# Performance work log

Measured on AMD Instinct MI355X. Metric: run time of the kernel, lower is better.

Reference implementation:

```python
import jax, jax.numpy as jnp
import numpy as np

N = 100_000   # nodes
E = 1_600_000 # edges
IN, HID, OUT = 128, 64, 32


def _glorot(key, fan_in, fan_out):
    s = jnp.sqrt(6.0 / (fan_in + fan_out)).astype(jnp.float32)
    return jax.random.uniform(key, (fan_in, fan_out), jnp.float32, -s, s)


def setup_inputs() -> dict:
    key = jax.random.key(0)
    ks = jax.random.split(key, 8)
    x = jax.random.normal(ks[0], (N, IN), jnp.float32)
    edge_index = jax.random.randint(ks[1], (2, E), 0, N, jnp.int64)
    return {
        "x": x,
        "edge_index": edge_index,
        "W1": _glorot(ks[2], IN, HID),
        "b1": jnp.zeros((HID,), jnp.float32),
        "W_mu": _glorot(ks[3], HID, OUT),
        "b_mu": jnp.zeros((OUT,), jnp.float32),
        "W_ls": _glorot(ks[4], HID, OUT),
        "b_ls": jnp.zeros((OUT,), jnp.float32),
    }


def _gcn_conv(x, W, b, src, dst, n, dinv_sqrt):
    """PyG GCNConv: h = x @ W; symmetric-normalized scatter-add incl. self-loops; + b."""
    h = x @ W                                       # [N, F_out]
    coef = dinv_sqrt[src] * dinv_sqrt[dst]          # [E]
    msg = h[src] * coef[:, None]                    # [E, F_out] gather
    agg = jax.ops.segment_sum(msg, dst, num_segments=n)  # scatter-add
    agg = agg + h * (dinv_sqrt * dinv_sqrt)[:, None]      # self-loop contribution
    return agg + b


def reference(x, edge_index, W1, b1, W_mu, b_mu, W_ls, b_ls):
    src, dst = edge_index[0], edge_index[1]
    n = x.shape[0]
    # degree on graph with self-loops (edge weight 1), shared by all three convs
    deg = jax.ops.segment_sum(jnp.ones((src.shape[0],), x.dtype), dst, num_segments=n) + 1.0
    dinv_sqrt = jax.lax.rsqrt(deg)
    h = jax.nn.relu(_gcn_conv(x, W1, b1, src, dst, n, dinv_sqrt))
    mu = _gcn_conv(h, W_mu, b_mu, src, dst, n, dinv_sqrt)
    logstd = _gcn_conv(h, W_ls, b_ls, src, dst, n, dinv_sqrt)
    return mu, logstd
```

## Files before the change

kernel.cpp:

```cpp
#include <hip/hip_runtime.h>
#include <hip/hip_bf16.h>

#define FIN 128
#define HID 64
#define BSN 128
#define BSHIFT 7
#define SRCBITS 20
#define EPB 2048
#define BSTRIDE 2304
#define STARTBITS 21

typedef __attribute__((ext_vector_type(8))) short short8;
typedef __attribute__((ext_vector_type(4))) float floatx4;

__device__ __forceinline__ float bf2f(unsigned short u) {
    union { unsigned int i; float f; } c;
    c.i = ((unsigned int)u) << 16;
    return c.f;
}

__device__ __forceinline__ unsigned short f2bf(float f) {
    union { float f; unsigned int i; } c;
    c.f = f;
    unsigned int u = c.i;
    unsigned int r = (u + 0x7FFFu + ((u >> 16) & 1u)) >> 16;
    return (unsigned short)r;
}

__global__ __launch_bounds__(256) void bin_fill(
    const int* __restrict__ src, const int* __restrict__ dst,
    int* __restrict__ bcur, unsigned* __restrict__ rec, int E) {
    __shared__ int hist[1024];
    __shared__ int cbase[1024];
    int t = threadIdx.x;
    for (int i = t; i < 1024; i += 256) hist[i] = 0;
    __syncthreads();
    int base = blockIdx.x * EPB;
    int lim = min(base + EPB, E);
    int d[8];
#pragma unroll
    for (int k = 0; k < 8; ++k) {
        int e = base + t + k * 256;
        if (e < lim) {
            d[k] = dst[e];
            atomicAdd(&hist[d[k] >> BSHIFT], 1);
        }
    }
    __syncthreads();
    for (int b = t; b < 1024; b += 256) {
        int c = hist[b];
        cbase[b] = c ? atomicAdd(&bcur[b], c) : 0;
    }
    __syncthreads();
    for (int i = t; i < 1024; i += 256) hist[i] = 0;
    __syncthreads();
#pragma unroll
    for (int k = 0; k < 8; ++k) {
        int e = base + t + k * 256;
        if (e < lim) {
            int dd = d[k];
            int bkt = dd >> BSHIFT;
            int slot = atomicAdd(&hist[bkt], 1);
            rec[bkt * BSTRIDE + cbase[bkt] + slot] =
                (unsigned)src[e] | ((unsigned)(dd & (BSN - 1)) << SRCBITS);
        }
    }
}

__global__ void csr_build(const unsigned* __restrict__ rec, const int* __restrict__ bcur,
                          unsigned* __restrict__ rowp, int* __restrict__ csr, int N) {
    __shared__ int cnt[BSN], excl[BSN], cur[BSN];
    int b = blockIdx.x, t = threadIdx.x;
    if (t < BSN) cnt[t] = 0;
    __syncthreads();
    int base = b * BSTRIDE;
    int cb = bcur[b];
    for (int i = t; i < cb; i += 256)
        atomicAdd(&cnt[rec[base + i] >> SRCBITS], 1);
    __syncthreads();
    if (t < BSN) excl[t] = cnt[t];
    __syncthreads();
    for (int off = 1; off < BSN; off <<= 1) {
        int a = 0;
        if (t < BSN && t >= off) a = excl[t - off];
        __syncthreads();
        if (t < BSN) excl[t] += a;
        __syncthreads();
    }
    if (t < BSN) {
        int inc = excl[t];
        int ex = inc - cnt[t];
        excl[t] = ex;
        cur[t] = 0;
        int n = b * BSN + t;
        if (n < N)
            rowp[n] = (unsigned)(base + ex) | ((unsigned)cnt[t] << STARTBITS);
    }
    __syncthreads();
    for (int i = t; i < cb; i += 256) {
        unsigned r = rec[base + i];
        int dl = r >> SRCBITS;
        int slot = atomicAdd(&cur[dl], 1);
        csr[base + excl[dl] + slot] = (int)(r & ((1u << SRCBITS) - 1));
    }
}

__global__ __launch_bounds__(256) void gemm1_mfma(
    const float* __restrict__ x, const float* __restrict__ W1,
    const unsigned* __restrict__ rowp, unsigned short* __restrict__ h0, int N) {
    __shared__ unsigned short Wt[64][136];
    {
        int t = threadIdx.x;
        int k  = t >> 1;
        int c0 = (t & 1) << 5;
        const float* wr = W1 + k * HID + c0;
#pragma unroll
        for (int cc = 0; cc < 32; ++cc)
            Wt[c0 + cc][k] = f2bf(wr[cc]);
    }
    __syncthreads();
    int wave = threadIdx.x >> 6, lane = threadIdx.x & 63;
    int m = lane & 15, q = lane >> 4;
    short8 bfr[4][4];
#pragma unroll
    for (int ct = 0; ct < 4; ++ct)
#pragma unroll
        for (int kk = 0; kk < 4; ++kk)
            bfr[ct][kk] = *((const short8*)&Wt[ct * 16 + m][kk * 32 + q * 8]);
    int ntiles = N >> 4;
    for (int t = blockIdx.x * 4 + wave; t < ntiles; t += gridDim.x * 4) {
        int nbase = t << 4;
        const float* xr = x + (size_t)(nbase + m) * FIN + q * 8;
        short8 afr[4];
#pragma unroll
        for (int kk = 0; kk < 4; ++kk) {
            float4 p0 = *((const float4*)(xr + kk * 32));
            float4 p1 = *((const float4*)(xr + kk * 32 + 4));
            short8 ta;
            ta[0] = (short)f2bf(p0.x); ta[1] = (short)f2bf(p0.y);
            ta[2] = (short)f2bf(p0.z); ta[3] = (short)f2bf(p0.w);
            ta[4] = (short)f2bf(p1.x); ta[5] = (short)f2bf(p1.y);
            ta[6] = (short)f2bf(p1.z); ta[7] = (short)f2bf(p1.w);
            afr[kk] = ta;
        }
        uint4 rp = *((const uint4*)(rowp + nbase + q * 4));
        floatx4 cacc[4];
#pragma unroll
        for (int ct = 0; ct < 4; ++ct) cacc[ct] = floatx4{0.f, 0.f, 0.f, 0.f};
#pragma unroll
        for (int ct = 0; ct < 4; ++ct)
#pragma unroll
            for (int kk = 0; kk < 4; ++kk)
                cacc[ct] = __builtin_amdgcn_mfma_f32_16x16x32_bf16(afr[kk], bfr[ct][kk], cacc[ct], 0, 0, 0);
#pragma unroll
        for (int ct = 0; ct < 4; ++ct) {
#pragma unroll
            for (int r = 0; r < 4; ++r) {
                unsigned pr = (r == 0) ? rp.x : (r == 1) ? rp.y : (r == 2) ? rp.z : rp.w;
                float d = rsqrtf((float)(pr >> STARTBITS) + 1.0f);
                int n = nbase + q * 4 + r;
                h0[(size_t)n * HID + ct * 16 + m] = f2bf(cacc[ct][r] * d);
            }
        }
    }
}


#define ACC8(a, d)                                                      \
    do {                                                                \
        union { unsigned u; float f; } c_;                              \
        c_.u = (d).x << 16;          a[0] += c_.f;                      \
        c_.u = (d).x & 0xFFFF0000u;  a[1] += c_.f;                      \
        c_.u = (d).y << 16;          a[2] += c_.f;                      \
        c_.u = (d).y & 0xFFFF0000u;  a[3] += c_.f;                      \
        c_.u = (d).z << 16;          a[4] += c_.f;                      \
        c_.u = (d).z & 0xFFFF0000u;  a[5] += c_.f;                      \
        c_.u = (d).w << 16;          a[6] += c_.f;                      \
        c_.u = (d).w & 0xFFFF0000u;  a[7] += c_.f;                      \
    } while (0)

template <int MODE>
__global__ __launch_bounds__(256, 4) void pull(
    const unsigned short* __restrict__ hp,
    const unsigned* __restrict__ rowp,
    const int* __restrict__ csr,
    const float* __restrict__ b1,
    unsigned short* __restrict__ outp,
    const float* __restrict__ Wmu, const float* __restrict__ bmu,
    const float* __restrict__ Wls, const float* __restrict__ bls,
    float* __restrict__ out, int N) {
    int lane = threadIdx.x & 63;
    int wave = threadIdx.x >> 6;
    int nd8  = lane >> 3;
    int g    = lane & 7;
    int n = blockIdx.x * 32 + wave * 8 + nd8;
    bool valid = (n < N);
    int nc = valid ? n : 0;
    unsigned rp = rowp[nc];
    int start = (int)(rp & ((1u << STARTBITS) - 1u));
    int deg   = (int)(rp >> STARTBITS);
    int end   = valid ? start + deg : 0;
    if (!valid) start = 0;
    const char* hpb = (const char*)hp;
    unsigned goff = (unsigned)(g << 4);
    uint4 sv = *((const uint4*)(hpb + (((unsigned)nc) << 7) + goff));
    float di = rsqrtf((float)deg + 1.0f);
    float4 bb0 = *((const float4*)(b1 + (g << 3)));
    float4 bb1 = *((const float4*)(b1 + (g << 3) + 4));
    float a[8] = {0.f, 0.f, 0.f, 0.f, 0.f, 0.f, 0.f, 0.f};
    int j = start;
    for (; j + 8 <= end; j += 8) {
        int s0 = csr[j],     s1 = csr[j + 1], s2 = csr[j + 2], s3 = csr[j + 3];
        int s4 = csr[j + 4], s5 = csr[j + 5], s6 = csr[j + 6], s7 = csr[j + 7];
        uint4 d0 = *((const uint4*)(hpb + (((unsigned)s0) << 7) + goff));
        uint4 d1 = *((const uint4*)(hpb + (((unsigned)s1) << 7) + goff));
        uint4 d2 = *((const uint4*)(hpb + (((unsigned)s2) << 7) + goff));
        uint4 d3 = *((const uint4*)(hpb + (((unsigned)s3) << 7) + goff));
        uint4 d4 = *((const uint4*)(hpb + (((unsigned)s4) << 7) + goff));
        uint4 d5 = *((const uint4*)(hpb + (((unsigned)s5) << 7) + goff));
        uint4 d6 = *((const uint4*)(hpb + (((unsigned)s6) << 7) + goff));
        uint4 d7 = *((const uint4*)(hpb + (((unsigned)s7) << 7) + goff));
        ACC8(a, d0); ACC8(a, d1); ACC8(a, d2); ACC8(a, d3);
        ACC8(a, d4); ACC8(a, d5); ACC8(a, d6); ACC8(a, d7);
    }
    if (j + 4 <= end) {
        int s0 = csr[j], s1 = csr[j + 1], s2 = csr[j + 2], s3 = csr[j + 3];
        uint4 d0 = *((const uint4*)(hpb + (((unsigned)s0) << 7) + goff));
        uint4 d1 = *((const uint4*)(hpb + (((unsigned)s1) << 7) + goff));
        uint4 d2 = *((const uint4*)(hpb + (((unsigned)s2) << 7) + goff));
        uint4 d3 = *((const uint4*)(hpb + (((unsigned)s3) << 7) + goff));
        ACC8(a, d0); ACC8(a, d1); ACC8(a, d2); ACC8(a, d3);
        j += 4;
    }
    if (j < end) {
        int i0 = j, i1 = min(j + 1, end - 1), i2 = min(j + 2, end - 1);
        int s0 = csr[i0], s1 = csr[i1], s2 = csr[i2];
        uint4 d0 = *((const uint4*)(hpb + (((unsigned)s0) << 7) + goff));
        uint4 d1 = *((const uint4*)(hpb + (((unsigned)s1) << 7) + goff));
        uint4 d2 = *((const uint4*)(hpb + (((unsigned)s2) << 7) + goff));
        if (j + 1 >= end) { d1.x = 0u; d1.y = 0u; d1.z = 0u; d1.w = 0u; }
        if (j + 2 >= end) { d2.x = 0u; d2.y = 0u; d2.z = 0u; d2.w = 0u; }
        ACC8(a, d0); ACC8(a, d1); ACC8(a, d2);
    }
    uint4 o = {0u, 0u, 0u, 0u};
    if (valid) {
        ACC8(a, sv);
        float v[8];
        if (MODE == 0) {
            float t0;
            t0 = di * a[0] + bb0.x; v[0] = (t0 > 0.f ? t0 : 0.f) * di;
            t0 = di * a[1] + bb0.y; v[1] = (t0 > 0.f ? t0 : 0.f) * di;
            t0 = di * a[2] + bb0.z; v[2] = (t0 > 0.f ? t0 : 0.f) * di;
            t0 = di * a[3] + bb0.w; v[3] = (t0 > 0.f ? t0 : 0.f) * di;
            t0 = di * a[4] + bb1.x; v[4] = (t0 > 0.f ? t0 : 0.f) * di;
            t0 = di * a[5] + bb1.y; v[5] = (t0 > 0.f ? t0 : 0.f) * di;
            t0 = di * a[6] + bb1.z; v[6] = (t0 > 0.f ? t0 : 0.f) * di;
            t0 = di * a[7] + bb1.w; v[7] = (t0 > 0.f ? t0 : 0.f) * di;
        } else {
#pragma unroll
            for (int k = 0; k < 8; ++k) v[k] = di * a[k];
        }
        o.x = (unsigned)f2bf(v[0]) | ((unsigned)f2bf(v[1]) << 16);
        o.y = (unsigned)f2bf(v[2]) | ((unsigned)f2bf(v[3]) << 16);
        o.z = (unsigned)f2bf(v[4]) | ((unsigned)f2bf(v[5]) << 16);
        o.w = (unsigned)f2bf(v[6]) | ((unsigned)f2bf(v[7]) << 16);
    }
    if constexpr (MODE == 0) {
        if (valid)
            *((uint4*)(outp + (size_t)n * HID + (g << 3))) = o;
    } else {
        __shared__ unsigned short ab[32][68];
        *((uint4*)&ab[wave * 8 + nd8][g << 3]) = o;
        __syncthreads();
        int m = lane & 15, q = lane >> 4;
        int tileId = wave >> 1;
        int ct0 = (wave & 1) * 2;
        short8 a0 = *((const short8*)&ab[tileId * 16 + m][q * 8]);
        short8 a1 = *((const short8*)&ab[tileId * 16 + m][32 + q * 8]);
        short8 bfr[2][2];
        float bias[2];
#pragma unroll
        for (int c = 0; c < 2; ++c) {
            int col = (ct0 + c) * 16 + m;
#pragma unroll
            for (int kk = 0; kk < 2; ++kk) {
                short8 tf;
#pragma unroll
                for (int jj = 0; jj < 8; ++jj) {
                    int k = kk * 32 + q * 8 + jj;
                    float w = (col < 32) ? Wmu[k * 32 + col] : Wls[k * 32 + (col - 32)];
                    tf[jj] = (short)f2bf(w);
                }
                bfr[c][kk] = tf;
            }
            bias[c] = (col < 32) ? bmu[col] : bls[col - 32];
        }
        floatx4 cc[2];
#pragma unroll
        for (int c = 0; c < 2; ++c) cc[c] = floatx4{0.f, 0.f, 0.f, 0.f};
#pragma unroll
        for (int c = 0; c < 2; ++c) {
            cc[c] = __builtin_amdgcn_mfma_f32_16x16x32_bf16(a0, bfr[c][0], cc[c], 0, 0, 0);
            cc[c] = __builtin_amdgcn_mfma_f32_16x16x32_bf16(a1, bfr[c][1], cc[c], 0, 0, 0);
        }
        int nb = blockIdx.x * 32 + tileId * 16;
#pragma unroll
        for (int c = 0; c < 2; ++c) {
            int col = (ct0 + c) * 16 + m;
            int which = col >> 5, oc = col & 31;
#pragma unroll
            for (int r = 0; r < 4; ++r) {
                int n2 = nb + q * 4 + r;
                if (n2 < N)
                    out[(size_t)which * N * 32 + (size_t)n2 * 32 + oc] = cc[c][r] + bias[c];
            }
        }
    }
}

extern "C" void kernel_launch(void* const* d_in, const int* in_sizes, int n_in,
                              void* d_out, int out_size, void* d_ws, size_t ws_size,
                              hipStream_t stream) {
    const float* x   = (const float*)d_in[0];
    const int*   ei  = (const int*)d_in[1];
    const float* W1  = (const float*)d_in[2];
    const float* b1  = (const float*)d_in[3];
    const float* Wmu = (const float*)d_in[4];
    const float* bmu = (const float*)d_in[5];
    const float* Wls = (const float*)d_in[6];
    const float* bls = (const float*)d_in[7];
    int N = in_sizes[0] / FIN;
    int E = in_sizes[1] / 2;
    const int* src = ei;
    const int* dst = ei + E;
    float* out = (float*)d_out;

    int B = (N + BSN - 1) / BSN;
    int nbin = (E + EPB - 1) / EPB;

    unsigned* rowp = (unsigned*)d_ws;
    int* bcur = (int*)(rowp + N);
    int* csr  = bcur + B;
    unsigned short* bufA = (unsigned short*)(csr + (size_t)B * BSTRIDE);
    char* region2 = (char*)(bufA + (size_t)N * HID);
    unsigned* rec        = (unsigned*)region2;
    unsigned short* bufB = (unsigned short*)region2;

    hipMemsetAsync(bcur, 0, (size_t)B * sizeof(int), stream);
    bin_fill<<<nbin, 256, 0, stream>>>(src, dst, bcur, rec, E);
    csr_build<<<B, 256, 0, stream>>>(rec, bcur, rowp, csr, N);

    gemm1_mfma<<<512, 256, 0, stream>>>(x, W1, rowp, bufA, N);

    int pgrid = (N + 31) / 32;
    pull<0><<<pgrid, 256, 0, stream>>>(bufA, rowp, csr, b1, bufB,
                                       Wmu, bmu, Wls, bls, out, N);
    pull<1><<<pgrid, 256, 0, stream>>>(bufB, rowp, csr, b1, (unsigned short*)0,
                                       Wmu, bmu, Wls, bls, out, N);
}
```

Measured before the change: 267.4 us.

## Fuse all stages into one cooperative persistent kernel with grid syncs

Merges the memset, binning, CSR build, first GEMM and both pull/aggregation stages into one cooperative kernel. The stages are separated by grid-wide barriers and run as grid-stride loops over a persistent grid sized from occupancy. The aim is to remove the launch overhead and inter-kernel gaps of six launches. In exchange, the fixed grid size (capped at 1024 blocks) may reduce parallelism in the edge-binning and pull stages, and each grid.sync adds its own cost. The multi-kernel path is kept as a fallback if the cooperative launch fails.

```diff
diff --git a/kernel.cpp b/kernel.cpp
--- a/kernel.cpp
+++ b/kernel.cpp
@@ -1,5 +1,8 @@
 #include <hip/hip_runtime.h>
 #include <hip/hip_bf16.h>
+#include <hip/hip_cooperative_groups.h>
+
+namespace cg = cooperative_groups;
 
 #define FIN 128
 #define HID 64
@@ -26,145 +29,6 @@
     unsigned int r = (u + 0x7FFFu + ((u >> 16) & 1u)) >> 16;
     return (unsigned short)r;
 }
-
-__global__ __launch_bounds__(256) void bin_fill(
-    const int* __restrict__ src, const int* __restrict__ dst,
-    int* __restrict__ bcur, unsigned* __restrict__ rec, int E) {
-    __shared__ int hist[1024];
-    __shared__ int cbase[1024];
-    int t = threadIdx.x;
-    for (int i = t; i < 1024; i += 256) hist[i] = 0;
-    __syncthreads();
-    int base = blockIdx.x * EPB;
-    int lim = min(base + EPB, E);
-    int d[8];
-#pragma unroll
-    for (int k = 0; k < 8; ++k) {
-        int e = base + t + k * 256;
-        if (e < lim) {
-            d[k] = dst[e];
-            atomicAdd(&hist[d[k] >> BSHIFT], 1);
-        }
-    }
-    __syncthreads();
-    for (int b = t; b < 1024; b += 256) {
-        int c = hist[b];
-        cbase[b] = c ? atomicAdd(&bcur[b], c) : 0;
-    }
-    __syncthreads();
-    for (int i = t; i < 1024; i += 256) hist[i] = 0;
-    __syncthreads();
-#pragma unroll
-    for (int k = 0; k < 8; ++k) {
-        int e = base + t + k * 256;
-        if (e < lim) {
-            int dd = d[k];
-            int bkt = dd >> BSHIFT;
-            int slot = atomicAdd(&hist[bkt], 1);
-            rec[bkt * BSTRIDE + cbase[bkt] + slot] =
-                (unsigned)src[e] | ((unsigned)(dd & (BSN - 1)) << SRCBITS);
-        }
-    }
-}
-
-__global__ void csr_build(const unsigned* __restrict__ rec, const int* __restrict__ bcur,
-                          unsigned* __restrict__ rowp, int* __restrict__ csr, int N) {
-    __shared__ int cnt[BSN], excl[BSN], cur[BSN];
-    int b = blockIdx.x, t = threadIdx.x;
-    if (t < BSN) cnt[t] = 0;
-    __syncthreads();
-    int base = b * BSTRIDE;
-    int cb = bcur[b];
-    for (int i = t; i < cb; i += 256)
-        atomicAdd(&cnt[rec[base + i] >> SRCBITS], 1);
-    __syncthreads();
-    if (t < BSN) excl[t] = cnt[t];
-    __syncthreads();
-    for (int off = 1; off < BSN; off <<= 1) {
-        int a = 0;
-        if (t < BSN && t >= off) a = excl[t - off];
-        __syncthreads();
-        if (t < BSN) excl[t] += a;
-        __syncthreads();
-    }
-    if (t < BSN) {
-        int inc = excl[t];
-        int ex = inc - cnt[t];
-        excl[t] = ex;
-        cur[t] = 0;
-        int n = b * BSN + t;
-        if (n < N)
-            rowp[n] = (unsigned)(base + ex) | ((unsigned)cnt[t] << STARTBITS);
-    }
-    __syncthreads();
-    for (int i = t; i < cb; i += 256) {
-        unsigned r = rec[base + i];
-        int dl = r >> SRCBITS;
-        int slot = atomicAdd(&cur[dl], 1);
-        csr[base + excl[dl] + slot] = (int)(r & ((1u << SRCBITS) - 1));
-    }
-}
-
-__global__ __launch_bounds__(256) void gemm1_mfma(
-    const float* __restrict__ x, const float* __restrict__ W1,
-    const unsigned* __restrict__ rowp, unsigned short* __restrict__ h0, int N) {
-    __shared__ unsigned short Wt[64][136];
-    {
-        int t = threadIdx.x;
-        int k  = t >> 1;
-        int c0 = (t & 1) << 5;
-        const float* wr = W1 + k * HID + c0;
-#pragma unroll
-        for (int cc = 0; cc < 32; ++cc)
-            Wt[c0 + cc][k] = f2bf(wr[cc]);
-    }
-    __syncthreads();
-    int wave = threadIdx.x >> 6, lane = threadIdx.x & 63;
-    int m = lane & 15, q = lane >> 4;
-    short8 bfr[4][4];
-#pragma unroll
-    for (int ct = 0; ct < 4; ++ct)
-#pragma unroll
-        for (int kk = 0; kk < 4; ++kk)
-            bfr[ct][kk] = *((const short8*)&Wt[ct * 16 + m][kk * 32 + q * 8]);
-    int ntiles = N >> 4;
-    for (int t = blockIdx.x * 4 + wave; t < ntiles; t += gridDim.x * 4) {
-        int nbase = t << 4;
-        const float* xr = x + (size_t)(nbase + m) * FIN + q * 8;
-        short8 afr[4];
-#pragma unroll
-        for (int kk = 0; kk < 4; ++kk) {
-            float4 p0 = *((const float4*)(xr + kk * 32));
-            float4 p1 = *((const float4*)(xr + kk * 32 + 4));
-            short8 ta;
-            ta[0] = (short)f2bf(p0.x); ta[1] = (short)f2bf(p0.y);
-            ta[2] = (short)f2bf(p0.z); ta[3] = (short)f2bf(p0.w);
-            ta[4] = (short)f2bf(p1.x); ta[5] = (short)f2bf(p1.y);
-            ta[6] = (short)f2bf(p1.z); ta[7] = (short)f2bf(p1.w);
-            afr[kk] = ta;
-        }
-        uint4 rp = *((const uint4*)(rowp + nbase + q * 4));
-        floatx4 cacc[4];
-#pragma unroll
-        for (int ct = 0; ct < 4; ++ct) cacc[ct] = floatx4{0.f, 0.f, 0.f, 0.f};
-#pragma unroll
-        for (int ct = 0; ct < 4; ++ct)
-#pragma unroll
-            for (int kk = 0; kk < 4; ++kk)
-                cacc[ct] = __builtin_amdgcn_mfma_f32_16x16x32_bf16(afr[kk], bfr[ct][kk], cacc[ct], 0, 0, 0);
-#pragma unroll
-        for (int ct = 0; ct < 4; ++ct) {
-#pragma unroll
-            for (int r = 0; r < 4; ++r) {
-                unsigned pr = (r == 0) ? rp.x : (r == 1) ? rp.y : (r == 2) ? rp.z : rp.w;
-                float d = rsqrtf((float)(pr >> STARTBITS) + 1.0f);
-                int n = nbase + q * 4 + r;
-                h0[(size_t)n * HID + ct * 16 + m] = f2bf(cacc[ct][r] * d);
-            }
-        }
-    }
-}
-
 
 #define ACC8(a, d)                                                      \
     do {                                                                \
@@ -178,6 +42,463 @@
         c_.u = (d).w << 16;          a[6] += c_.f;                      \
         c_.u = (d).w & 0xFFFF0000u;  a[7] += c_.f;                      \
     } while (0)
+
+__device__ __forceinline__ void gather_node(
+    const char* hpb, const unsigned* __restrict__ rowp,
+    const int* __restrict__ csr, int nc, bool valid, unsigned goff,
+    float a[8], float& di, uint4& sv) {
+    unsigned rp = rowp[nc];
+    int start = (int)(rp & ((1u << STARTBITS) - 1u));
+    int deg   = (int)(rp >> STARTBITS);
+    int end   = valid ? start + deg : 0;
+    if (!valid) start = 0;
+    sv = *((const uint4*)(hpb + (((unsigned)nc) << 7) + goff));
+    di = rsqrtf((float)deg + 1.0f);
+    int j = start;
+    for (; j + 8 <= end; j += 8) {
+        int s0 = csr[j],     s1 = csr[j + 1], s2 = csr[j + 2], s3 = csr[j + 3];
+        int s4 = csr[j + 4], s5 = csr[j + 5], s6 = csr[j + 6], s7 = csr[j + 7];
+        uint4 d0 = *((const uint4*)(hpb + (((unsigned)s0) << 7) + goff));
+        uint4 d1 = *((const uint4*)(hpb + (((unsigned)s1) << 7) + goff));
+        uint4 d2 = *((const uint4*)(hpb + (((unsigned)s2) << 7) + goff));
+        uint4 d3 = *((const uint4*)(hpb + (((unsigned)s3) << 7) + goff));
+        uint4 d4 = *((const uint4*)(hpb + (((unsigned)s4) << 7) + goff));
+        uint4 d5 = *((const uint4*)(hpb + (((unsigned)s5) << 7) + goff));
+        uint4 d6 = *((const uint4*)(hpb + (((unsigned)s6) << 7) + goff));
+        uint4 d7 = *((const uint4*)(hpb + (((unsigned)s7) << 7) + goff));
+        ACC8(a, d0); ACC8(a, d1); ACC8(a, d2); ACC8(a, d3);
+        ACC8(a, d4); ACC8(a, d5); ACC8(a, d6); ACC8(a, d7);
+    }
+    if (j + 4 <= end) {
+        int s0 = csr[j], s1 = csr[j + 1], s2 = csr[j + 2], s3 = csr[j + 3];
+        uint4 d0 = *((const uint4*)(hpb + (((unsigned)s0) << 7) + goff));
+        uint4 d1 = *((const uint4*)(hpb + (((unsigned)s1) << 7) + goff));
+        uint4 d2 = *((const uint4*)(hpb + (((unsigned)s2) << 7) + goff));
+        uint4 d3 = *((const uint4*)(hpb + (((unsigned)s3) << 7) + goff));
+        ACC8(a, d0); ACC8(a, d1); ACC8(a, d2); ACC8(a, d3);
+        j += 4;
+    }
+    if (j < end) {
+        int i0 = j, i1 = min(j + 1, end - 1), i2 = min(j + 2, end - 1);
+        int s0 = csr[i0], s1 = csr[i1], s2 = csr[i2];
+        uint4 d0 = *((const uint4*)(hpb + (((unsigned)s0) << 7) + goff));
+        uint4 d1 = *((const uint4*)(hpb + (((unsigned)s1) << 7) + goff));
+        uint4 d2 = *((const uint4*)(hpb + (((unsigned)s2) << 7) + goff));
+        if (j + 1 >= end) { d1.x = 0u; d1.y = 0u; d1.z = 0u; d1.w = 0u; }
+        if (j + 2 >= end) { d2.x = 0u; d2.y = 0u; d2.z = 0u; d2.w = 0u; }
+        ACC8(a, d0); ACC8(a, d1); ACC8(a, d2);
+    }
+}
+
+__global__ __launch_bounds__(256, 4) void fused_all(
+    const int* __restrict__ src, const int* __restrict__ dst,
+    const float* __restrict__ x, const float* __restrict__ W1,
+    const float* __restrict__ b1,
+    const float* __restrict__ Wmu, const float* __restrict__ bmu,
+    const float* __restrict__ Wls, const float* __restrict__ bls,
+    float* __restrict__ out,
+    unsigned* __restrict__ rowp, int* __restrict__ bcur, int* __restrict__ csr,
+    unsigned short* __restrict__ bufA, unsigned* __restrict__ rec,
+    unsigned short* __restrict__ bufB, int N, int E) {
+    cg::grid_group gridg = cg::this_grid();
+    const int bid = blockIdx.x, t = threadIdx.x;
+    const int lane = t & 63, wave = t >> 6;
+    const int nd8 = lane >> 3, g = lane & 7;
+    const int B = (N + BSN - 1) / BSN;
+    const int nbin = (E + EPB - 1) / EPB;
+
+    __shared__ __align__(16) char smem[17408];
+
+    for (int i = bid * 256 + t; i < B; i += gridDim.x * 256) bcur[i] = 0;
+    gridg.sync();
+
+    {
+        int* hist  = (int*)smem;
+        int* cbase = hist + 1024;
+        for (int blk = bid; blk < nbin; blk += gridDim.x) {
+            for (int i = t; i < 1024; i += 256) hist[i] = 0;
+            __syncthreads();
+            int base = blk * EPB;
+            int lim = min(base + EPB, E);
+            int d[8];
+#pragma unroll
+            for (int k = 0; k < 8; ++k) {
+                int e = base + t + k * 256;
+                if (e < lim) {
+                    d[k] = dst[e];
+                    atomicAdd(&hist[d[k] >> BSHIFT], 1);
+                }
+            }
+            __syncthreads();
+            for (int b = t; b < 1024; b += 256) {
+                int c = hist[b];
+                cbase[b] = c ? atomicAdd(&bcur[b], c) : 0;
+            }
+            __syncthreads();
+            for (int i = t; i < 1024; i += 256) hist[i] = 0;
+            __syncthreads();
+#pragma unroll
+            for (int k = 0; k < 8; ++k) {
+                int e = base + t + k * 256;
+                if (e < lim) {
+                    int dd = d[k];
+                    int bkt = dd >> BSHIFT;
+                    int slot = atomicAdd(&hist[bkt], 1);
+                    rec[bkt * BSTRIDE + cbase[bkt] + slot] =
+                        (unsigned)src[e] | ((unsigned)(dd & (BSN - 1)) << SRCBITS);
+                }
+            }
+            __syncthreads();
+        }
+    }
+    gridg.sync();
+
+    {
+        int* cnt  = (int*)smem;
+        int* excl = cnt + BSN;
+        int* cur  = excl + BSN;
+        for (int blk = bid; blk < B; blk += gridDim.x) {
+            if (t < BSN) cnt[t] = 0;
+            __syncthreads();
+            int base = blk * BSTRIDE;
+            int cb = bcur[blk];
+            for (int i = t; i < cb; i += 256)
+                atomicAdd(&cnt[rec[base + i] >> SRCBITS], 1);
+            __syncthreads();
+            if (t < BSN) excl[t] = cnt[t];
+            __syncthreads();
+            for (int off = 1; off < BSN; off <<= 1) {
+                int a = 0;
+                if (t < BSN && t >= off) a = excl[t - off];
+                __syncthreads();
+                if (t < BSN) excl[t] += a;
+                __syncthreads();
+            }
+            if (t < BSN) {
+                int inc = excl[t];
+                int ex = inc - cnt[t];
+                excl[t] = ex;
+                cur[t] = 0;
+                int n = blk * BSN + t;
+                if (n < N)
+                    rowp[n] = (unsigned)(base + ex) | ((unsigned)cnt[t] << STARTBITS);
+            }
+            __syncthreads();
+            for (int i = t; i < cb; i += 256) {
+                unsigned r = rec[base + i];
+                int dl = r >> SRCBITS;
+                int slot = atomicAdd(&cur[dl], 1);
+                csr[base + excl[dl] + slot] = (int)(r & ((1u << SRCBITS) - 1));
+            }
+            __syncthreads();
+        }
+    }
+    gridg.sync();
+
+    {
+        typedef unsigned short WtRow[136];
+        WtRow* Wt = (WtRow*)smem;
+        {
+            int k  = t >> 1;
+            int c0 = (t & 1) << 5;
+            const float* wr = W1 + k * HID + c0;
+#pragma unroll
+            for (int cc = 0; cc < 32; ++cc)
+                Wt[c0 + cc][k] = f2bf(wr[cc]);
+        }
+        __syncthreads();
+        int m = lane & 15, q = lane >> 4;
+        short8 bfr[4][4];
+#pragma unroll
+        for (int ct = 0; ct < 4; ++ct)
+#pragma unroll
+            for (int kk = 0; kk < 4; ++kk)
+                bfr[ct][kk] = *((const short8*)&Wt[ct * 16 + m][kk * 32 + q * 8]);
+        int ntiles = N >> 4;
+        for (int tt = bid * 4 + wave; tt < ntiles; tt += gridDim.x * 4) {
+            int nbase = tt << 4;
+            const float* xr = x + (size_t)(nbase + m) * FIN + q * 8;
+            short8 afr[4];
+#pragma unroll
+            for (int kk = 0; kk < 4; ++kk) {
+                float4 p0 = *((const float4*)(xr + kk * 32));
+                float4 p1 = *((const float4*)(xr + kk * 32 + 4));
+                short8 ta;
+                ta[0] = (short)f2bf(p0.x); ta[1] = (short)f2bf(p0.y);
+                ta[2] = (short)f2bf(p0.z); ta[3] = (short)f2bf(p0.w);
+                ta[4] = (short)f2bf(p1.x); ta[5] = (short)f2bf(p1.y);
+                ta[6] = (short)f2bf(p1.z); ta[7] = (short)f2bf(p1.w);
+                afr[kk] = ta;
+            }
+            uint4 rp = *((const uint4*)(rowp + nbase + q * 4));
+            floatx4 cacc[4];
+#pragma unroll
+            for (int ct = 0; ct < 4; ++ct) cacc[ct] = floatx4{0.f, 0.f, 0.f, 0.f};
+#pragma unroll
+            for (int ct = 0; ct < 4; ++ct)
+#pragma unroll
+                for (int kk = 0; kk < 4; ++kk)
+                    cacc[ct] = __builtin_amdgcn_mfma_f32_16x16x32_bf16(afr[kk], bfr[ct][kk], cacc[ct], 0, 0, 0);
+#pragma unroll
+            for (int ct = 0; ct < 4; ++ct) {
+#pragma unroll
+                for (int r = 0; r < 4; ++r) {
+                    unsigned pr = (r == 0) ? rp.x : (r == 1) ? rp.y : (r == 2) ? rp.z : rp.w;
+                    float d = rsqrtf((float)(pr >> STARTBITS) + 1.0f);
+                    int n = nbase + q * 4 + r;
+                    bufA[(size_t)n * HID + ct * 16 + m] = f2bf(cacc[ct][r] * d);
+                }
+            }
+        }
+    }
+    gridg.sync();
+
+    {
+        const char* hpb = (const char*)bufA;
+        unsigned goff = (unsigned)(g << 4);
+        float4 bb0 = *((const float4*)(b1 + (g << 3)));
+        float4 bb1 = *((const float4*)(b1 + (g << 3) + 4));
+        int pgrid = (N + 31) / 32;
+        for (int vb = bid; vb < pgrid; vb += gridDim.x) {
+            int n = vb * 32 + wave * 8 + nd8;
+            bool valid = (n < N);
+            int nc = valid ? n : 0;
+            float a[8] = {0.f, 0.f, 0.f, 0.f, 0.f, 0.f, 0.f, 0.f};
+            float di; uint4 sv;
+            gather_node(hpb, rowp, csr, nc, valid, goff, a, di, sv);
+            if (valid) {
+                ACC8(a, sv);
+                float v[8], t0;
+                t0 = di * a[0] + bb0.x; v[0] = (t0 > 0.f ? t0 : 0.f) * di;
+                t0 = di * a[1] + bb0.y; v[1] = (t0 > 0.f ? t0 : 0.f) * di;
+                t0 = di * a[2] + bb0.z; v[2] = (t0 > 0.f ? t0 : 0.f) * di;
+                t0 = di * a[3] + bb0.w; v[3] = (t0 > 0.f ? t0 : 0.f) * di;
+                t0 = di * a[4] + bb1.x; v[4] = (t0 > 0.f ? t0 : 0.f) * di;
+                t0 = di * a[5] + bb1.y; v[5] = (t0 > 0.f ? t0 : 0.f) * di;
+                t0 = di * a[6] + bb1.z; v[6] = (t0 > 0.f ? t0 : 0.f) * di;
+                t0 = di * a[7] + bb1.w; v[7] = (t0 > 0.f ? t0 : 0.f) * di;
+                uint4 o;
+                o.x = (unsigned)f2bf(v[0]) | ((unsigned)f2bf(v[1]) << 16);
+                o.y = (unsigned)f2bf(v[2]) | ((unsigned)f2bf(v[3]) << 16);
+                o.z = (unsigned)f2bf(v[4]) | ((unsigned)f2bf(v[5]) << 16);
+                o.w = (unsigned)f2bf(v[6]) | ((unsigned)f2bf(v[7]) << 16);
+                *((uint4*)(bufB + (size_t)n * HID + (g << 3))) = o;
+            }
+        }
+    }
+    gridg.sync();
+
+    {
+        typedef unsigned short AbRow[68];
+        AbRow* ab = (AbRow*)smem;
+        const char* hpb = (const char*)bufB;
+        unsigned goff = (unsigned)(g << 4);
+        int m = lane & 15, q = lane >> 4;
+        int tileId = wave >> 1;
+        int ct0 = (wave & 1) * 2;
+        short8 wfr[2][2];
+        float wbias[2];
+#pragma unroll
+        for (int c = 0; c < 2; ++c) {
+            int col = (ct0 + c) * 16 + m;
+#pragma unroll
+            for (int kk = 0; kk < 2; ++kk) {
+                short8 tf;
+#pragma unroll
+                for (int jj = 0; jj < 8; ++jj) {
+                    int k = kk * 32 + q * 8 + jj;
+                    float w = (col < 32) ? Wmu[k * 32 + col] : Wls[k * 32 + (col - 32)];
+                    tf[jj] = (short)f2bf(w);
+                }
+                wfr[c][kk] = tf;
+            }
+            wbias[c] = (col < 32) ? bmu[col] : bls[col - 32];
+        }
+        int pgrid = (N + 31) / 32;
+        for (int vb = bid; vb < pgrid; vb += gridDim.x) {
+            __syncthreads();
+            int n = vb * 32 + wave * 8 + nd8;
+            bool valid = (n < N);
+            int nc = valid ? n : 0;
+            float a[8] = {0.f, 0.f, 0.f, 0.f, 0.f, 0.f, 0.f, 0.f};
+            float di; uint4 sv;
+            gather_node(hpb, rowp, csr, nc, valid, goff, a, di, sv);
+            uint4 o = {0u, 0u, 0u, 0u};
+            if (valid) {
+                ACC8(a, sv);
+                float v[8];
+#pragma unroll
+                for (int k = 0; k < 8; ++k) v[k] = di * a[k];
+                o.x = (unsigned)f2bf(v[0]) | ((unsigned)f2bf(v[1]) << 16);
+                o.y = (unsigned)f2bf(v[2]) | ((unsigned)f2bf(v[3]) << 16);
+                o.z = (unsigned)f2bf(v[4]) | ((unsigned)f2bf(v[5]) << 16);
+                o.w = (unsigned)f2bf(v[6]) | ((unsigned)f2bf(v[7]) << 16);
+            }
+            *((uint4*)&ab[wave * 8 + nd8][g << 3]) = o;
+            __syncthreads();
+            short8 a0 = *((const short8*)&ab[tileId * 16 + m][q * 8]);
+            short8 a1 = *((const short8*)&ab[tileId * 16 + m][32 + q * 8]);
+            floatx4 cc[2];
+#pragma unroll
+            for (int c = 0; c < 2; ++c) cc[c] = floatx4{0.f, 0.f, 0.f, 0.f};
+#pragma unroll
+            for (int c = 0; c < 2; ++c) {
+                cc[c] = __builtin_amdgcn_mfma_f32_16x16x32_bf16(a0, wfr[c][0], cc[c], 0, 0, 0);
+                cc[c] = __builtin_amdgcn_mfma_f32_16x16x32_bf16(a1, wfr[c][1], cc[c], 0, 0, 0);
+            }
+            int nb = vb * 32 + tileId * 16;
+#pragma unroll
+            for (int c = 0; c < 2; ++c) {
+                int col = (ct0 + c) * 16 + m;
+                int which = col >> 5, oc = col & 31;
+#pragma unroll
+                for (int r = 0; r < 4; ++r) {
+                    int n2 = nb + q * 4 + r;
+                    if (n2 < N)
+                        out[(size_t)which * N * 32 + (size_t)n2 * 32 + oc] = cc[c][r] + wbias[c];
+                }
+            }
+        }
+    }
+}
+
+__global__ __launch_bounds__(256) void bin_fill(
+    const int* __restrict__ src, const int* __restrict__ dst,
+    int* __restrict__ bcur, unsigned* __restrict__ rec, int E) {
+    __shared__ int hist[1024];
+    __shared__ int cbase[1024];
+    int t = threadIdx.x;
+    for (int i = t; i < 1024; i += 256) hist[i] = 0;
+    __syncthreads();
+    int base = blockIdx.x * EPB;
+    int lim = min(base + EPB, E);
+    int d[8];
+#pragma unroll
+    for (int k = 0; k < 8; ++k) {
+        int e = base + t + k * 256;
+        if (e < lim) {
+            d[k] = dst[e];
+            atomicAdd(&hist[d[k] >> BSHIFT], 1);
+        }
+    }
+    __syncthreads();
+    for (int b = t; b < 1024; b += 256) {
+        int c = hist[b];
+        cbase[b] = c ? atomicAdd(&bcur[b], c) : 0;
+    }
+    __syncthreads();
+    for (int i = t; i < 1024; i += 256) hist[i] = 0;
+    __syncthreads();
+#pragma unroll
+    for (int k = 0; k < 8; ++k) {
+        int e = base + t + k * 256;
+        if (e < lim) {
+            int dd = d[k];
+            int bkt = dd >> BSHIFT;
+            int slot = atomicAdd(&hist[bkt], 1);
+            rec[bkt * BSTRIDE + cbase[bkt] + slot] =
+                (unsigned)src[e] | ((unsigned)(dd & (BSN - 1)) << SRCBITS);
+        }
+    }
+}
+
+__global__ void csr_build(const unsigned* __restrict__ rec, const int* __restrict__ bcur,
+                          unsigned* __restrict__ rowp, int* __restrict__ csr, int N) {
+    __shared__ int cnt[BSN], excl[BSN], cur[BSN];
+    int b = blockIdx.x, t = threadIdx.x;
+    if (t < BSN) cnt[t] = 0;
+    __syncthreads();
+    int base = b * BSTRIDE;
+    int cb = bcur[b];
+    for (int i = t; i < cb; i += 256)
+        atomicAdd(&cnt[rec[base + i] >> SRCBITS], 1);
+    __syncthreads();
+    if (t < BSN) excl[t] = cnt[t];
+    __syncthreads();
+    for (int off = 1; off < BSN; off <<= 1) {
+        int a = 0;
+        if (t < BSN && t >= off) a = excl[t - off];
+        __syncthreads();
+        if (t < BSN) excl[t] += a;
+        __syncthreads();
+    }
+    if (t < BSN) {
+        int inc = excl[t];
+        int ex = inc - cnt[t];
+        excl[t] = ex;
+        cur[t] = 0;
+        int n = b * BSN + t;
+        if (n < N)
+            rowp[n] = (unsigned)(base + ex) | ((unsigned)cnt[t] << STARTBITS);
+    }
+    __syncthreads();
+    for (int i = t; i < cb; i += 256) {
+        unsigned r = rec[base + i];
+        int dl = r >> SRCBITS;
+        int slot = atomicAdd(&cur[dl], 1);
+        csr[base + excl[dl] + slot] = (int)(r & ((1u << SRCBITS) - 1));
+    }
+}
+
+__global__ __launch_bounds__(256) void gemm1_mfma(
+    const float* __restrict__ x, const float* __restrict__ W1,
+    const unsigned* __restrict__ rowp, unsigned short* __restrict__ h0, int N) {
+    __shared__ unsigned short Wt[64][136];
+    {
+        int t = threadIdx.x;
+        int k  = t >> 1;
+        int c0 = (t & 1) << 5;
+        const float* wr = W1 + k * HID + c0;
+#pragma unroll
+        for (int cc = 0; cc < 32; ++cc)
+            Wt[c0 + cc][k] = f2bf(wr[cc]);
+    }
+    __syncthreads();
+    int wave = threadIdx.x >> 6, lane = threadIdx.x & 63;
+    int m = lane & 15, q = lane >> 4;
+    short8 bfr[4][4];
+#pragma unroll
+    for (int ct = 0; ct < 4; ++ct)
+#pragma unroll
+        for (int kk = 0; kk < 4; ++kk)
+            bfr[ct][kk] = *((const short8*)&Wt[ct * 16 + m][kk * 32 + q * 8]);
+    int ntiles = N >> 4;
+    for (int t = blockIdx.x * 4 + wave; t < ntiles; t += gridDim.x * 4) {
+        int nbase = t << 4;
+        const float* xr = x + (size_t)(nbase + m) * FIN + q * 8;
+        short8 afr[4];
+#pragma unroll
+        for (int kk = 0; kk < 4; ++kk) {
+            float4 p0 = *((const float4*)(xr + kk * 32));
+            float4 p1 = *((const float4*)(xr + kk * 32 + 4));
+            short8 ta;
+            ta[0] = (short)f2bf(p0.x); ta[1] = (short)f2bf(p0.y);
+            ta[2] = (short)f2bf(p0.z); ta[3] = (short)f2bf(p0.w);
+            ta[4] = (short)f2bf(p1.x); ta[5] = (short)f2bf(p1.y);
+            ta[6] = (short)f2bf(p1.z); ta[7] = (short)f2bf(p1.w);
+            afr[kk] = ta;
+        }
+        uint4 rp = *((const uint4*)(rowp + nbase + q * 4));
+        floatx4 cacc[4];
+#pragma unroll
+        for (int ct = 0; ct < 4; ++ct) cacc[ct] = floatx4{0.f, 0.f, 0.f, 0.f};
+#pragma unroll
+        for (int ct = 0; ct < 4; ++ct)
+#pragma unroll
+            for (int kk = 0; kk < 4; ++kk)
+                cacc[ct] = __builtin_amdgcn_mfma_f32_16x16x32_bf16(afr[kk], bfr[ct][kk], cacc[ct], 0, 0, 0);
+#pragma unroll
+        for (int ct = 0; ct < 4; ++ct) {
+#pragma unroll
+            for (int r = 0; r < 4; ++r) {
+                unsigned pr = (r == 0) ? rp.x : (r == 1) ? rp.y : (r == 2) ? rp.z : rp.w;
+                float d = rsqrtf((float)(pr >> STARTBITS) + 1.0f);
+                int n = nbase + q * 4 + r;
+                h0[(size_t)n * HID + ct * 16 + m] = f2bf(cacc[ct][r] * d);
+            }
+        }
+    }
+}
 
 template <int MODE>
 __global__ __launch_bounds__(256, 4) void pull(
@@ -196,57 +517,18 @@
     int n = blockIdx.x * 32 + wave * 8 + nd8;
     bool valid = (n < N);
     int nc = valid ? n : 0;
-    unsigned rp = rowp[nc];
-    int start = (int)(rp & ((1u << STARTBITS) - 1u));
-    int deg   = (int)(rp >> STARTBITS);
-    int end   = valid ? start + deg : 0;
-    if (!valid) start = 0;
     const char* hpb = (const char*)hp;
     unsigned goff = (unsigned)(g << 4);
-    uint4 sv = *((const uint4*)(hpb + (((unsigned)nc) << 7) + goff));
-    float di = rsqrtf((float)deg + 1.0f);
-    float4 bb0 = *((const float4*)(b1 + (g << 3)));
-    float4 bb1 = *((const float4*)(b1 + (g << 3) + 4));
     float a[8] = {0.f, 0.f, 0.f, 0.f, 0.f, 0.f, 0.f, 0.f};
-    int j = start;
-    for (; j + 8 <= end; j += 8) {
-        int s0 = csr[j],     s1 = csr[j + 1], s2 = csr[j + 2], s3 = csr[j + 3];
-        int s4 = csr[j + 4], s5 = csr[j + 5], s6 = csr[j + 6], s7 = csr[j + 7];
-        uint4 d0 = *((const uint4*)(hpb + (((unsigned)s0) << 7) + goff));
-        uint4 d1 = *((const uint4*)(hpb + (((unsigned)s1) << 7) + goff));
-        uint4 d2 = *((const uint4*)(hpb + (((unsigned)s2) << 7) + goff));
-        uint4 d3 = *((const uint4*)(hpb + (((unsigned)s3) << 7) + goff));
-        uint4 d4 = *((const uint4*)(hpb + (((unsigned)s4) << 7) + goff));
-        uint4 d5 = *((const uint4*)(hpb + (((unsigned)s5) << 7) + goff));
-        uint4 d6 = *((const uint4*)(hpb + (((unsigned)s6) << 7) + goff));
-        uint4 d7 = *((const uint4*)(hpb + (((unsigned)s7) << 7) + goff));
-        ACC8(a, d0); ACC8(a, d1); ACC8(a, d2); ACC8(a, d3);
-        ACC8(a, d4); ACC8(a, d5); ACC8(a, d6); ACC8(a, d7);
-    }
-    if (j + 4 <= end) {
-        int s0 = csr[j], s1 = csr[j + 1], s2 = csr[j + 2], s3 = csr[j + 3];
-        uint4 d0 = *((const uint4*)(hpb + (((unsigned)s0) << 7) + goff));
-        uint4 d1 = *((const uint4*)(hpb + (((unsigned)s1) << 7) + goff));
-        uint4 d2 = *((const uint4*)(hpb + (((unsigned)s2) << 7) + goff));
-        uint4 d3 = *((const uint4*)(hpb + (((unsigned)s3) << 7) + goff));
-        ACC8(a, d0); ACC8(a, d1); ACC8(a, d2); ACC8(a, d3);
-        j += 4;
-    }
-    if (j < end) {
-        int i0 = j, i1 = min(j + 1, end - 1), i2 = min(j + 2, end - 1);
-        int s0 = csr[i0], s1 = csr[i1], s2 = csr[i2];
-        uint4 d0 = *((const uint4*)(hpb + (((unsigned)s0) << 7) + goff));
-        uint4 d1 = *((const uint4*)(hpb + (((unsigned)s1) << 7) + goff));
-        uint4 d2 = *((const uint4*)(hpb + (((unsigned)s2) << 7) + goff));
-        if (j + 1 >= end) { d1.x = 0u; d1.y = 0u; d1.z = 0u; d1.w = 0u; }
-        if (j + 2 >= end) { d2.x = 0u; d2.y = 0u; d2.z = 0u; d2.w = 0u; }
-        ACC8(a, d0); ACC8(a, d1); ACC8(a, d2);
-    }
+    float di; uint4 sv;
+    gather_node(hpb, rowp, csr, nc, valid, goff, a, di, sv);
     uint4 o = {0u, 0u, 0u, 0u};
     if (valid) {
         ACC8(a, sv);
         float v[8];
         if (MODE == 0) {
+            float4 bb0 = *((const float4*)(b1 + (g << 3)));
+            float4 bb1 = *((const float4*)(b1 + (g << 3) + 4));
             float t0;
             t0 = di * a[0] + bb0.x; v[0] = (t0 > 0.f ? t0 : 0.f) * di;
             t0 = di * a[1] + bb0.y; v[1] = (t0 > 0.f ? t0 : 0.f) * di;
@@ -336,7 +618,6 @@
     float* out = (float*)d_out;
 
     int B = (N + BSN - 1) / BSN;
-    int nbin = (E + EPB - 1) / EPB;
 
     unsigned* rowp = (unsigned*)d_ws;
     int* bcur = (int*)(rowp + N);
@@ -346,12 +627,32 @@
     unsigned* rec        = (unsigned*)region2;
     unsigned short* bufB = (unsigned short*)region2;
 
+    static int g_grid = -2;
+    if (g_grid == -2) {
+        int maxb = 0;
+        if (hipOccupancyMaxActiveBlocksPerMultiprocessor(
+                &maxb, (const void*)fused_all, 256, 0) != hipSuccess)
+            maxb = 0;
+        g_grid = maxb * 256;
+        if (g_grid > 1024) g_grid = 1024;
+    }
+    if (g_grid >= 256) {
+        void* args[] = {
+            (void*)&src, (void*)&dst, (void*)&x, (void*)&W1, (void*)&b1,
+            (void*)&Wmu, (void*)&bmu, (void*)&Wls, (void*)&bls, (void*)&out,
+            (void*)&rowp, (void*)&bcur, (void*)&csr, (void*)&bufA,
+            (void*)&rec, (void*)&bufB, (void*)&N, (void*)&E};
+        hipError_t e = hipLaunchCooperativeKernel(
+            (const void*)fused_all, dim3(g_grid), dim3(256), args, 0, stream);
+        if (e == hipSuccess) return;
+        g_grid = 0;
+    }
+
+    int nbin = (E + EPB - 1) / EPB;
     hipMemsetAsync(bcur, 0, (size_t)B * sizeof(int), stream);
     bin_fill<<<nbin, 256, 0, stream>>>(src, dst, bcur, rec, E);
     csr_build<<<B, 256, 0, stream>>>(rec, bcur, rowp, csr, N);
-
     gemm1_mfma<<<512, 256, 0, stream>>>(x, W1, rowp, bufA, N);
-
     int pgrid = (N + 31) / 32;
     pull<0><<<pgrid, 256, 0, stream>>>(bufA, rowp, csr, b1, bufB,
                                        Wmu, bmu, Wls, bls, out, N);
```

Result: slower. 572.3 us (+114.0%).

## Split hidden features into two 32-wide planes and gather each plane separately

Applied to the files above, without the earlier changes.

The 64-wide bf16 hidden features are now stored as two separate [N,32] planes instead of interleaved rows. The pull kernel runs the neighbour gather twice, once per plane, reading 8-byte chunks instead of 16-byte ones. The aim is to make each gather pass touch a smaller working set that fits better in cache, improving hit rate for the random row accesses. The cost is walking the CSR indices twice and issuing twice as many smaller load instructions, which can raise latency and instruction overhead.

```diff
diff --git a/kernel.cpp b/kernel.cpp
--- a/kernel.cpp
+++ b/kernel.cpp
@@ -154,29 +154,27 @@
                 cacc[ct] = __builtin_amdgcn_mfma_f32_16x16x32_bf16(afr[kk], bfr[ct][kk], cacc[ct], 0, 0, 0);
 #pragma unroll
         for (int ct = 0; ct < 4; ++ct) {
+            int f = ct * 16 + m;
+            size_t hbase = (size_t)(f >> 5) * N * 32 + (f & 31);
 #pragma unroll
             for (int r = 0; r < 4; ++r) {
                 unsigned pr = (r == 0) ? rp.x : (r == 1) ? rp.y : (r == 2) ? rp.z : rp.w;
                 float d = rsqrtf((float)(pr >> STARTBITS) + 1.0f);
                 int n = nbase + q * 4 + r;
-                h0[(size_t)n * HID + ct * 16 + m] = f2bf(cacc[ct][r] * d);
+                h0[hbase + (size_t)n * 32] = f2bf(cacc[ct][r] * d);
             }
         }
     }
 }
 
 
-#define ACC8(a, d)                                                      \
+#define ACC4(a, d)                                                      \
     do {                                                                \
         union { unsigned u; float f; } c_;                              \
         c_.u = (d).x << 16;          a[0] += c_.f;                      \
         c_.u = (d).x & 0xFFFF0000u;  a[1] += c_.f;                      \
         c_.u = (d).y << 16;          a[2] += c_.f;                      \
         c_.u = (d).y & 0xFFFF0000u;  a[3] += c_.f;                      \
-        c_.u = (d).z << 16;          a[4] += c_.f;                      \
-        c_.u = (d).z & 0xFFFF0000u;  a[5] += c_.f;                      \
-        c_.u = (d).w << 16;          a[6] += c_.f;                      \
-        c_.u = (d).w & 0xFFFF0000u;  a[7] += c_.f;                      \
     } while (0)
 
 template <int MODE>
@@ -189,6 +187,7 @@
     const float* __restrict__ Wmu, const float* __restrict__ bmu,
     const float* __restrict__ Wls, const float* __restrict__ bls,
     float* __restrict__ out, int N) {
+    __shared__ unsigned short ab[32][68];
     int lane = threadIdx.x & 63;
     int wave = threadIdx.x >> 6;
     int nd8  = lane >> 3;
@@ -201,76 +200,75 @@
     int deg   = (int)(rp >> STARTBITS);
     int end   = valid ? start + deg : 0;
     if (!valid) start = 0;
-    const char* hpb = (const char*)hp;
-    unsigned goff = (unsigned)(g << 4);
-    uint4 sv = *((const uint4*)(hpb + (((unsigned)nc) << 7) + goff));
     float di = rsqrtf((float)deg + 1.0f);
-    float4 bb0 = *((const float4*)(b1 + (g << 3)));
-    float4 bb1 = *((const float4*)(b1 + (g << 3) + 4));
-    float a[8] = {0.f, 0.f, 0.f, 0.f, 0.f, 0.f, 0.f, 0.f};
-    int j = start;
-    for (; j + 8 <= end; j += 8) {
-        int s0 = csr[j],     s1 = csr[j + 1], s2 = csr[j + 2], s3 = csr[j + 3];
-        int s4 = csr[j + 4], s5 = csr[j + 5], s6 = csr[j + 6], s7 = csr[j + 7];
-        uint4 d0 = *((const uint4*)(hpb + (((unsigned)s0) << 7) + goff));
-        uint4 d1 = *((const uint4*)(hpb + (((unsigned)s1) << 7) + goff));
-        uint4 d2 = *((const uint4*)(hpb + (((unsigned)s2) << 7) + goff));
-        uint4 d3 = *((const uint4*)(hpb + (((unsigned)s3) << 7) + goff));
-        uint4 d4 = *((const uint4*)(hpb + (((unsigned)s4) << 7) + goff));
-        uint4 d5 = *((const uint4*)(hpb + (((unsigned)s5) << 7) + goff));
-        uint4 d6 = *((const uint4*)(hpb + (((unsigned)s6) << 7) + goff));
-        uint4 d7 = *((const uint4*)(hpb + (((unsigned)s7) << 7) + goff));
-        ACC8(a, d0); ACC8(a, d1); ACC8(a, d2); ACC8(a, d3);
-        ACC8(a, d4); ACC8(a, d5); ACC8(a, d6); ACC8(a, d7);
-    }
-    if (j + 4 <= end) {
-        int s0 = csr[j], s1 = csr[j + 1], s2 = csr[j + 2], s3 = csr[j + 3];
-        uint4 d0 = *((const uint4*)(hpb + (((unsigned)s0) << 7) + goff));
-        uint4 d1 = *((const uint4*)(hpb + (((unsigned)s1) << 7) + goff));
-        uint4 d2 = *((const uint4*)(hpb + (((unsigned)s2) << 7) + goff));
-        uint4 d3 = *((const uint4*)(hpb + (((unsigned)s3) << 7) + goff));
-        ACC8(a, d0); ACC8(a, d1); ACC8(a, d2); ACC8(a, d3);
-        j += 4;
-    }
-    if (j < end) {
-        int i0 = j, i1 = min(j + 1, end - 1), i2 = min(j + 2, end - 1);
-        int s0 = csr[i0], s1 = csr[i1], s2 = csr[i2];
-        uint4 d0 = *((const uint4*)(hpb + (((unsigned)s0) << 7) + goff));
-        uint4 d1 = *((const uint4*)(hpb + (((unsigned)s1) << 7) + goff));
-        uint4 d2 = *((const uint4*)(hpb + (((unsigned)s2) << 7) + goff));
-        if (j + 1 >= end) { d1.x = 0u; d1.y = 0u; d1.z = 0u; d1.w = 0u; }
-        if (j + 2 >= end) { d2.x = 0u; d2.y = 0u; d2.z = 0u; d2.w = 0u; }
-        ACC8(a, d0); ACC8(a, d1); ACC8(a, d2);
-    }
-    uint4 o = {0u, 0u, 0u, 0u};
-    if (valid) {
-        ACC8(a, sv);
-        float v[8];
-        if (MODE == 0) {
-            float t0;
-            t0 = di * a[0] + bb0.x; v[0] = (t0 > 0.f ? t0 : 0.f) * di;
-            t0 = di * a[1] + bb0.y; v[1] = (t0 > 0.f ? t0 : 0.f) * di;
-            t0 = di * a[2] + bb0.z; v[2] = (t0 > 0.f ? t0 : 0.f) * di;
-            t0 = di * a[3] + bb0.w; v[3] = (t0 > 0.f ? t0 : 0.f) * di;
-            t0 = di * a[4] + bb1.x; v[4] = (t0 > 0.f ? t0 : 0.f) * di;
-            t0 = di * a[5] + bb1.y; v[5] = (t0 > 0.f ? t0 : 0.f) * di;
-            t0 = di * a[6] + bb1.z; v[6] = (t0 > 0.f ? t0 : 0.f) * di;
-            t0 = di * a[7] + bb1.w; v[7] = (t0 > 0.f ? t0 : 0.f) * di;
+    unsigned goff = (unsigned)(g << 3);
+
+#pragma unroll
+    for (int h = 0; h < 2; ++h) {
+        const char* hpb = (const char*)(hp + (size_t)h * N * 32);
+        uint2 sv = *((const uint2*)(hpb + (((unsigned)nc) << 6) + goff));
+        float4 bb = *((const float4*)(b1 + h * 32 + (g << 2)));
+        float a[4] = {0.f, 0.f, 0.f, 0.f};
+        int j = start;
+        for (; j + 8 <= end; j += 8) {
+            int s0 = csr[j],     s1 = csr[j + 1], s2 = csr[j + 2], s3 = csr[j + 3];
+            int s4 = csr[j + 4], s5 = csr[j + 5], s6 = csr[j + 6], s7 = csr[j + 7];
+            uint2 d0 = *((const uint2*)(hpb + (((unsigned)s0) << 6) + goff));
+            uint2 d1 = *((const uint2*)(hpb + (((unsigned)s1) << 6) + goff));
+            uint2 d2 = *((const uint2*)(hpb + (((unsigned)s2) << 6) + goff));
+            uint2 d3 = *((const uint2*)(hpb + (((unsigned)s3) << 6) + goff));
+            uint2 d4 = *((const uint2*)(hpb + (((unsigned)s4) << 6) + goff));
+            uint2 d5 = *((const uint2*)(hpb + (((unsigned)s5) << 6) + goff));
+            uint2 d6 = *((const uint2*)(hpb + (((unsigned)s6) << 6) + goff));
+            uint2 d7 = *((const uint2*)(hpb + (((unsigned)s7) << 6) + goff));
+            ACC4(a, d0); ACC4(a, d1); ACC4(a, d2); ACC4(a, d3);
+            ACC4(a, d4); ACC4(a, d5); ACC4(a, d6); ACC4(a, d7);
+        }
+        if (j + 4 <= end) {
+            int s0 = csr[j], s1 = csr[j + 1], s2 = csr[j + 2], s3 = csr[j + 3];
+            uint2 d0 = *((const uint2*)(hpb + (((unsigned)s0) << 6) + goff));
+            uint2 d1 = *((const uint2*)(hpb + (((unsigned)s1) << 6) + goff));
+            uint2 d2 = *((const uint2*)(hpb + (((unsigned)s2) << 6) + goff));
+            uint2 d3 = *((const uint2*)(hpb + (((unsigned)s3) << 6) + goff));
+            ACC4(a, d0); ACC4(a, d1); ACC4(a, d2); ACC4(a, d3);
+            j += 4;
+        }
+        if (j < end) {
+            int i0 = j, i1 = min(j + 1, end - 1), i2 = min(j + 2, end - 1);
+            int s0 = csr[i0], s1 = csr[i1], s2 = csr[i2];
+            uint2 d0 = *((const uint2*)(hpb + (((unsigned)s0) << 6) + goff));
+            uint2 d1 = *((const uint2*)(hpb + (((unsigned)s1) << 6) + goff));
+            uint2 d2 = *((const uint2*)(hpb + (((unsigned)s2) << 6) + goff));
+            if (j + 1 >= end) { d1.x = 0u; d1.y = 0u; }
+            if (j + 2 >= end) { d2.x = 0u; d2.y = 0u; }
+            ACC4(a, d0); ACC4(a, d1); ACC4(a, d2);
+        }
+        uint2 o = {0u, 0u};
+        if (valid) {
+            ACC4(a, sv);
+            float v[4];
+            if (MODE == 0) {
+                float t0;
+                t0 = di * a[0] + bb.x; v[0] = (t0 > 0.f ? t0 : 0.f) * di;
+                t0 = di * a[1] + bb.y; v[1] = (t0 > 0.f ? t0 : 0.f) * di;
+                t0 = di * a[2] + bb.z; v[2] = (t0 > 0.f ? t0 : 0.f) * di;
+                t0 = di * a[3] + bb.w; v[3] = (t0 > 0.f ? t0 : 0.f) * di;
+            } else {
+#pragma unroll
+                for (int k = 0; k < 4; ++k) v[k] = di * a[k];
+            }
+            o.x = (unsigned)f2bf(v[0]) | ((unsigned)f2bf(v[1]) << 16);
+            o.y = (unsigned)f2bf(v[2]) | ((unsigned)f2bf(v[3]) << 16);
+        }
+        if constexpr (MODE == 0) {
+            if (valid)
+                *((uint2*)(outp + (size_t)h * N * 32 + (size_t)n * 32 + (g << 2))) = o;
         } else {
-#pragma unroll
-            for (int k = 0; k < 8; ++k) v[k] = di * a[k];
-        }
-        o.x = (unsigned)f2bf(v[0]) | ((unsigned)f2bf(v[1]) << 16);
-        o.y = (unsigned)f2bf(v[2]) | ((unsigned)f2bf(v[3]) << 16);
-        o.z = (unsigned)f2bf(v[4]) | ((unsigned)f2bf(v[5]) << 16);
-        o.w = (unsigned)f2bf(v[6]) | ((unsigned)f2bf(v[7]) << 16);
-    }
-    if constexpr (MODE == 0) {
-        if (valid)
-            *((uint4*)(outp + (size_t)n * HID + (g << 3))) = o;
-    } else {
-        __shared__ unsigned short ab[32][68];
-        *((uint4*)&ab[wave * 8 + nd8][g << 3]) = o;
+            *((uint2*)&ab[wave * 8 + nd8][h * 32 + (g << 2)]) = o;
+        }
+    }
+
+    if constexpr (MODE == 1) {
         __syncthreads();
         int m = lane & 15, q = lane >> 4;
         int tileId = wave >> 1;
```

Measured after the change: 301.1 us. 1.13x slower.
